# Kernel tuning notes

Measured on AMD Instinct MI355X. Metric: run time of the kernel, lower is better.

The kernel has to match this reference:

```python
import jax, jax.numpy as jnp
import numpy as np

N = 16384
K = 8

def knn_indices(pos, k):
    # squared pairwise distances via ||a||^2 + ||b||^2 - 2 a.b  -> [N, N]
    sq = jnp.sum(pos * pos, axis=-1)
    d = sq[:, None] + sq[None, :] - 2.0 * (pos @ pos.T)
    n = pos.shape[0]
    d = d.at[jnp.arange(n), jnp.arange(n)].set(jnp.inf)  # exclude self (loop=False)
    _, idx = jax.lax.top_k(-d, k)  # k nearest neighbors per target node
    # PointNetConv adds self-loops by default -> append self index
    return jnp.concatenate([idx, jnp.arange(n)[:, None]], axis=1)  # [N, k+1]

def mlp(x, W1, b1, W2, b2):
    return jax.nn.relu(x @ W1 + b1) @ W2 + b2

def pointnet_conv(x, pos, idx, W1, b1, W2, b2):
    # message: concat(x_j, pos_j - pos_i); aggregate: max over neighbors
    rel = pos[idx] - pos[:, None, :]                 # [N, k+1, 3]
    msg = jnp.concatenate([x[idx], rel], axis=-1)    # [N, k+1, d+3]
    h = mlp(msg, W1, b1, W2, b2)                     # [N, k+1, d_out]
    return jnp.max(h, axis=1)                        # [N, d_out]

def setup_inputs() -> dict:
    key = jax.random.key(0)
    ks = jax.random.split(key, 11)
    def lin(k, fi, fo):
        kw, kb = jax.random.split(k)
        s = 1.0 / np.sqrt(fi)
        return (jax.random.uniform(kw, (fi, fo), jnp.float32, -s, s),
                jax.random.uniform(kb, (fo,), jnp.float32, -s, s))
    W1a, b1a = lin(ks[0], 6, 32)
    W1b, b1b = lin(ks[1], 32, 64)
    W2a, b2a = lin(ks[2], 67, 64)
    W2b, b2b = lin(ks[3], 64, 128)
    Wc, bc = lin(ks[4], 128, 5)
    pos = jax.random.normal(ks[5], (N, 3), jnp.float32)
    return {"pos": pos, "W1a": W1a, "b1a": b1a, "W1b": W1b, "b1b": b1b,
            "W2a": W2a, "b2a": b2a, "W2b": W2b, "b2b": b2b, "Wc": Wc, "bc": bc}

def reference(pos, W1a, b1a, W1b, b1b, W2a, b2a, W2b, b2b, Wc, bc):
    idx = knn_indices(pos, K)                                    # [N, K+1]
    x = jax.nn.relu(pointnet_conv(pos, pos, idx, W1a, b1a, W1b, b1b))  # [N, 64]
    x = jax.nn.relu(pointnet_conv(x, pos, idx, W2a, b2a, W2b, b2b))    # [N, 128]
    logits = x @ Wc + bc                                         # [N, 5]
    return jax.nn.log_softmax(logits, axis=-1)
```

## Files before the change

kernel.cpp:

```cpp
#include <hip/hip_runtime.h>
#include <hip/hip_bf16.h>
#include <math.h>

#define N_PTS 16384
#define KNN 8

#define DT_BF16 1
#define DT_FP32 2

#define WS_FLAG_OFF 0
#define WS_IDX_OFF  64
#define WS_X1_OFF   589888
#define WS_NEEDED   4784192

#define WS_SAT_OFF      (WS_X1_OFF)
#define WS_START_OFF    (WS_X1_OFF + 442368)
#define WS_CURSOR_OFF   (WS_X1_OFF + 884800)
#define WS_PID_OFF      (WS_X1_OFF + 1327168)
#define WS_PTS_OFF      (WS_X1_OFF + 1392704)
#define WS_ROWTOT_OFF   (WS_X1_OFF + 1654848)
#define WS_ROWSTART_OFF (WS_X1_OFF + 1664064)
#define WS_XPRE_OFF     (WS_X1_OFF + 1673280)

#define GRID_R   48
#define NROWS2D  (GRID_R * GRID_R)
#define NCELLS   (GRID_R * GRID_R * GRID_R)
#define GLO      -4.5f
#define CELL_E   0.1875f
#define CELL_INV 5.3333335f
#define NBR_MIN  40
#define NBR_LO   9
#define M_CAP    1024
#define R_DIRECT 96

#define SENT_KEY 0xFF800000FFFFFFFFull

__device__ __forceinline__ float bf2f(__hip_bfloat16 v) { return __bfloat162float(v); }

__device__ __forceinline__ float ldf(const float* p, int i) { return p[i]; }
__device__ __forceinline__ float ldf(const __hip_bfloat16* p, int i) { return bf2f(p[i]); }
__device__ __forceinline__ void stf(float* p, int i, float v) { p[i] = v; }
__device__ __forceinline__ void stf(__hip_bfloat16* p, int i, float v) { p[i] = __float2bfloat16(v); }

__device__ __forceinline__ int clamp_idx(int j) {
    return ((unsigned)j < (unsigned)N_PTS) ? j : 0;
}

__device__ __forceinline__ int cell_of(float v) {
    int c = (int)((v - GLO) * CELL_INV);
    return min(max(c, 0), GRID_R - 1);
}

__device__ __forceinline__ unsigned fkey(float d) {
    unsigned b = __float_as_uint(d);
    return b ^ ((unsigned)((int)b >> 31) | 0x80000000u);
}
__device__ __forceinline__ float fkey_inv(unsigned k) {
    unsigned b = (k & 0x80000000u) ? (k ^ 0x80000000u) : ~k;
    return __uint_as_float(b);
}

__device__ __forceinline__ int get_dt(const int* flag) {
    return (flag[0] > 16) ? DT_FP32 : DT_BF16;
}

__global__ __launch_bounds__(256) void zero_kernel(int* __restrict__ cnt, int* __restrict__ flag) {
    const int e = blockIdx.x * 256 + threadIdx.x;
    cnt[e] = 0;
    if (e == 0) flag[0] = 0;
}

__global__ __launch_bounds__(256) void sniff_kernel(const unsigned short* __restrict__ posu,
                                                    int* __restrict__ flag) {
    __shared__ int red[256];
    int local = 0;
    for (int e = blockIdx.x * 256 + threadIdx.x; e < 3 * N_PTS; e += 64 * 256) {
        const float v = __uint_as_float(((unsigned)posu[e]) << 16);
        if (!(fabsf(v) <= 64.0f)) local++;
    }
    red[threadIdx.x] = local;
    __syncthreads();
    for (int s = 128; s > 0; s >>= 1) {
        if (threadIdx.x < s) red[threadIdx.x] += red[threadIdx.x + s];
        __syncthreads();
    }
    if (threadIdx.x == 0 && red[0] > 0) atomicAdd(flag, red[0]);
}

template <typename T>
__device__ __forceinline__ void count_body(const T* __restrict__ pos, int* __restrict__ cnt) {
    const int i = blockIdx.x * 256 + threadIdx.x;
    const float x = ldf(pos, 3 * i + 0);
    const float y = ldf(pos, 3 * i + 1);
    const float z = ldf(pos, 3 * i + 2);
    const int c = (cell_of(z) * GRID_R + cell_of(y)) * GRID_R + cell_of(x);
    atomicAdd(&cnt[c], 1);
}

__global__ __launch_bounds__(256) void grid_count_kernel(const void* __restrict__ pos,
                                                         const int* __restrict__ flag,
                                                         int* __restrict__ cnt) {
    if (get_dt(flag) == DT_BF16) count_body<__hip_bfloat16>((const __hip_bfloat16*)pos, cnt);
    else                         count_body<float>((const float*)pos, cnt);
}

__global__ __launch_bounds__(256) void rowscan_kernel(int* __restrict__ sat,
                                                      int* __restrict__ xpre,
                                                      int* __restrict__ rowtot) {
    const int t = blockIdx.x * 256 + threadIdx.x;
    const int rb = t * GRID_R;
    int acc = 0;
    for (int x = 0; x < GRID_R; ++x) {
        acc += sat[rb + x];
        sat[rb + x]  = acc;
        xpre[rb + x] = acc;
    }
    rowtot[t] = acc;
}

__global__ __launch_bounds__(256) void rowoffset_kernel(const int* __restrict__ rowtot,
                                                        int* __restrict__ rowstart) {
    __shared__ int part[256];
    const int t = threadIdx.x;
    int loc[9]; int s = 0;
#pragma unroll
    for (int k = 0; k < 9; ++k) { loc[k] = rowtot[t * 9 + k]; s += loc[k]; }
    part[t] = s;
    __syncthreads();
    for (int off = 1; off < 256; off <<= 1) {
        int v = (t >= off) ? part[t - off] : 0;
        __syncthreads();
        part[t] += v;
        __syncthreads();
    }
    int run = (t == 0) ? 0 : part[t - 1];
#pragma unroll
    for (int k = 0; k < 9; ++k) { rowstart[t * 9 + k] = run; run += loc[k]; }
}

__global__ __launch_bounds__(256) void cellsaty_kernel(const int* __restrict__ xpre,
                                                       const int* __restrict__ rowstart,
                                                       int* __restrict__ cstart,
                                                       int* __restrict__ cursor,
                                                       int* __restrict__ sat) {
    const int t = blockIdx.x * 256 + threadIdx.x;
    const int rb = t * GRID_R;
    const int base = rowstart[t];
    int prev = 0;
    for (int x = 0; x < GRID_R; ++x) {
        const int v = base + prev;
        cstart[rb + x] = v;
        cursor[rb + x] = v;
        prev = xpre[rb + x];
    }
    if (t == NROWS2D - 1) cstart[NCELLS] = base + prev;
    const int z = t / GRID_R, x = t - z * GRID_R;
    const int b2 = z * NROWS2D + x;
    int run = 0;
#pragma unroll
    for (int y = 0; y < GRID_R; ++y) {
        run += sat[b2 + y * GRID_R];
        sat[b2 + y * GRID_R] = run;
    }
}

template <typename T>
__device__ __forceinline__ void scatter_body(const T* __restrict__ pos, int i,
                                             int* __restrict__ cursor,
                                             float4* __restrict__ pts4, int* __restrict__ pid) {
    const float x = ldf(pos, 3 * i + 0);
    const float y = ldf(pos, 3 * i + 1);
    const float z = ldf(pos, 3 * i + 2);
    const int c = (cell_of(z) * GRID_R + cell_of(y)) * GRID_R + cell_of(x);
    const int slot = atomicAdd(&cursor[c], 1);
    const float sq = fmaf(x, x, fmaf(y, y, z * z));
    pts4[slot] = make_float4(-2.0f * x, -2.0f * y, -2.0f * z, sq);
    pid[slot] = i;
}

__global__ __launch_bounds__(256) void satzscatter_kernel(const void* __restrict__ pos,
                                                          const int* __restrict__ flag,
                                                          int* __restrict__ sat,
                                                          int* __restrict__ cursor,
                                                          float4* __restrict__ pts4,
                                                          int* __restrict__ pid) {
    if (blockIdx.x < 9) {
        const int t = blockIdx.x * 256 + threadIdx.x;
        int run = 0;
#pragma unroll
        for (int z = 0; z < GRID_R; ++z) {
            run += sat[t + z * NROWS2D];
            sat[t + z * NROWS2D] = run;
        }
    } else {
        const int i = (blockIdx.x - 9) * 256 + threadIdx.x;
        if (get_dt(flag) == DT_BF16) scatter_body<__hip_bfloat16>((const __hip_bfloat16*)pos, i, cursor, pts4, pid);
        else                         scatter_body<float>((const float*)pos, i, cursor, pts4, pid);
    }
}

__device__ __forceinline__ int sat_at(const int* __restrict__ sat, int x, int y, int z) {
    if (x < 0 || y < 0 || z < 0) return 0;
    return sat[(z * GRID_R + y) * GRID_R + x];
}

__device__ __forceinline__ int boxcount(const int* __restrict__ sat,
                                        int x0, int x1, int y0, int y1, int z0, int z1) {
    return sat_at(sat, x1, y1, z1) - sat_at(sat, x0 - 1, y1, z1)
         - sat_at(sat, x1, y0 - 1, z1) - sat_at(sat, x1, y1, z0 - 1)
         + sat_at(sat, x0 - 1, y0 - 1, z1) + sat_at(sat, x0 - 1, y1, z0 - 1)
         + sat_at(sat, x1, y0 - 1, z0 - 1) - sat_at(sat, x0 - 1, y0 - 1, z0 - 1);
}

template <typename T>
__device__ void knn_body(const T* __restrict__ pos,
                         const int* __restrict__ cstart, const int* __restrict__ sat,
                         const float4* __restrict__ pts4, const int* __restrict__ pid,
                         int* __restrict__ idx_out,
                         int* __restrict__ rs, int* __restrict__ epf) {
    const int tid  = threadIdx.x;
    const int lane = tid & 31;
    const int i    = blockIdx.x * 8 + (tid >> 5);

    const float pix = ldf(pos, 3 * i + 0);
    const float piy = ldf(pos, 3 * i + 1);
    const float piz = ldf(pos, 3 * i + 2);
    const float sqi = fmaf(pix, pix, fmaf(piy, piy, piz * piz));
    const int cx = cell_of(pix), cy = cell_of(piy), cz = cell_of(piz);

    unsigned long long bk[KNN];
#pragma unroll
    for (int q = 0; q < KNN; ++q) bk[q] = SENT_KEY;
    unsigned long long tk = SENT_KEY;

    auto do_insert = [&](unsigned long long ck) {
#pragma unroll
        for (int q = 0; q < KNN; ++q) {
            const unsigned long long old = bk[q];
            const bool ins = ck < old;
            bk[q] = ins ? ck : old;
            ck    = ins ? old : ck;
        }
        tk = (bk[KNN - 1] < tk) ? bk[KNN - 1] : tk;
    };

    auto clip_row = [&](int ycell, int zcell, float clip2, bool doclip,
                        int x0, int x1, int& cxa, int& cxb) -> bool {
        cxa = x0; cxb = x1;
        if (doclip) {
            const float ylo = GLO + (float)ycell * CELL_E;
            const float zlo = GLO + (float)zcell * CELL_E;
            const float dy = fmaxf(0.0f, fmaxf(ylo - piy, piy - (ylo + CELL_E)));
            const float dz = fmaxf(0.0f, fmaxf(zlo - piz, piz - (zlo + CELL_E)));
            const float rad2 = clip2 - dy * dy - dz * dz;
            if (rad2 <= 0.0f) return false;
            const float hr = sqrtf(rad2) + 1e-4f;
            cxa = max(x0, (int)floorf((pix - hr - GLO) * CELL_INV));
            cxb = min(x1, (int)floorf((pix + hr - GLO) * CELL_INV));
        }
        return cxa <= cxb;
    };

    auto cand_key = [&](int si) -> unsigned long long {
        const float4 cq = pts4[si];
        const int pj = pid[si];
        const float d = fmaf(cq.x, pix, fmaf(cq.y, piy, fmaf(cq.z, piz, cq.w)));
        if (pj == i) return SENT_KEY;
        return ((unsigned long long)fkey(d) << 32) | (unsigned)pj;
    };

    auto scan_win = [&](int rr, float clipR) {
        const int x0 = max(cx - rr, 0), x1 = min(cx + rr, GRID_R - 1);
        const int y0 = max(cy - rr, 0), y1 = min(cy + rr, GRID_R - 1);
        const int z0 = max(cz - rr, 0), z1 = min(cz + rr, GRID_R - 1);
        const int ny = y1 - y0 + 1;
        const int nz = z1 - z0 + 1;
        const int R  = ny * nz;
        const float clip2 = clipR * clipR;
        const bool doclip = (clipR < 1e30f);

        if (R > R_DIRECT) {
            for (int t0 = lane; t0 < R; t0 += 128) {
                int s0v[4], s1v[4];
#pragma unroll
                for (int k = 0; k < 4; ++k) {
                    const int row = t0 + (k << 5);
                    s0v[k] = 0; s1v[k] = 0;
                    if (row < R) {
                        const int iz = row / ny;
                        const int iy = row - iz * ny;
                        int cxa, cxb;
                        if (clip_row(y0 + iy, z0 + iz, clip2, doclip, x0, x1, cxa, cxb)) {
                            const int c0 = ((z0 + iz) * GRID_R + (y0 + iy)) * GRID_R + cxa;
                            s0v[k] = cstart[c0];
                            s1v[k] = cstart[c0 + (cxb - cxa) + 1];
                        }
                    }
                }
#pragma unroll
                for (int k = 0; k < 4; ++k) {
                    for (int si = s0v[k]; si < s1v[k]; ++si) {
                        const unsigned long long ck = cand_key(si);
                        if (ck <= tk) do_insert(ck);
                    }
                }
            }
            return;
        }

        for (int cb = 0; cb < R; cb += 32) {
            const int lr = cb + lane;
            int cnt_r = 0, st_r = 0;
            if (lr < R) {
                const int izq = lr / ny;
                const int iyq = lr - izq * ny;
                int cxa, cxb;
                if (clip_row(y0 + iyq, z0 + izq, clip2, doclip, x0, x1, cxa, cxb)) {
                    const int c0 = ((z0 + izq) * GRID_R + (y0 + iyq)) * GRID_R + cxa;
                    st_r  = cstart[c0];
                    cnt_r = cstart[c0 + (cxb - cxa) + 1] - st_r;
                }
            }
            int pv = cnt_r;
#pragma unroll
            for (int s = 1; s < 32; s <<= 1) {
                const int u = __shfl_up(pv, s, 32);
                if (lane >= s) pv += u;
            }
            const int Mtot = __shfl(pv, 31, 32);
            asm volatile("s_waitcnt lgkmcnt(0)" ::: "memory");
            rs[lane]  = st_r;
            epf[lane] = (lr < R) ? (pv - cnt_r) : 0x7fffffff;
            asm volatile("s_waitcnt lgkmcnt(0)" ::: "memory");
            for (int tb = 0; tb < Mtot; tb += 128) {
                unsigned long long ck[4];
#pragma unroll
                for (int k = 0; k < 4; ++k) {
                    const int t = tb + (k << 5) + lane;
                    ck[k] = SENT_KEY;
                    if (t < Mtot) {
                        int p = 0;
#pragma unroll
                        for (int st = 16; st >= 1; st >>= 1)
                            if (epf[p + st] <= t) p += st;
                        ck[k] = cand_key(rs[p] + (t - epf[p]));
                    }
                }
#pragma unroll
                for (int k = 0; k < 4; ++k)
                    if (ck[k] <= tk) do_insert(ck[k]);
            }
        }
    };

    auto merge_all = [&]() {
#pragma unroll
        for (int s = 1; s < 32; s <<= 1) {
            unsigned long long m[KNN];
#pragma unroll
            for (int q = 0; q < KNN; ++q) {
                const unsigned long long o = __shfl_xor(bk[KNN - 1 - q], s, 32);
                m[q] = (bk[q] < o) ? bk[q] : o;
            }
#pragma unroll
            for (int d = 4; d >= 1; d >>= 1) {
#pragma unroll
                for (int q = 0; q < KNN; ++q) {
                    if (!(q & d)) {
                        const unsigned long long a = m[q], b = m[q + d];
                        const bool sw = b < a;
                        m[q]     = sw ? b : a;
                        m[q + d] = sw ? a : b;
                    }
                }
            }
#pragma unroll
            for (int q = 0; q < KNN; ++q) bk[q] = m[q];
        }
        tk = bk[KNN - 1];
    };

    int r;
    {
        const int rl = lane + 1;
        const int bx0 = max(cx - rl, 0), bx1 = min(cx + rl, GRID_R - 1);
        const int by0 = max(cy - rl, 0), by1 = min(cy + rl, GRID_R - 1);
        const int bz0 = max(cz - rl, 0), bz1 = min(cz + rl, GRID_R - 1);
        const int cntl = boxcount(sat, bx0, bx1, by0, by1, bz0, bz1);
        const unsigned long long m9  = __ballot(cntl >= NBR_LO);
        const unsigned long long m26 = __ballot(cntl >= NBR_MIN);
        const unsigned sh  = (unsigned)(tid & 32);
        const unsigned mh9  = (unsigned)(m9  >> sh);
        const unsigned mh26 = (unsigned)(m26 >> sh);
        const int r9  = mh9  ? (int)__ffs(mh9)  : 32;
        const int r26 = mh26 ? (int)__ffs(mh26) : 32;
        const int cnt26 = __shfl(cntl, r26 - 1, 32);
        r = (cnt26 <= M_CAP) ? r26 : r9;
    }

    scan_win(r, INFINITY);

    {
        float mg = INFINITY;
        bool full = true;
        if (cx - r > 0)          { mg = fminf(mg, pix - (GLO + (float)(cx - r) * CELL_E));     full = false; }
        if (cx + r < GRID_R - 1) { mg = fminf(mg, (GLO + (float)(cx + r + 1) * CELL_E) - pix); full = false; }
        if (cy - r > 0)          { mg = fminf(mg, piy - (GLO + (float)(cy - r) * CELL_E));     full = false; }
        if (cy + r < GRID_R - 1) { mg = fminf(mg, (GLO + (float)(cy + r + 1) * CELL_E) - piy); full = false; }
        if (cz - r > 0)          { mg = fminf(mg, piz - (GLO + (float)(cz - r) * CELL_E));     full = false; }
        if (cz + r < GRID_R - 1) { mg = fminf(mg, (GLO + (float)(cz + r + 1) * CELL_E) - piz); full = false; }

        merge_all();
        bool done = full;
        const unsigned long long d8key = bk[KNN - 1];
        const float d8 = fkey_inv((unsigned)(d8key >> 32));
        if (!full) {
            const float mge  = mg - 1e-5f;
            const float need = mge * mge - sqi;
            done = (d8 < need);
        }

        if (!done) {
            float s2 = sqrtf(fmaxf(d8 + sqi, 0.0f)) + 1e-4f;
            s2 = fminf(s2, 9.0f);
            auto dneed = [&](float frac, int clip) -> int {
                int nd = (int)ceilf((s2 - frac) * CELL_INV);
                nd = max(nd, 0);
                return min(nd, clip);
            };
            const float fxm = pix - (GLO + (float)cx * CELL_E);
            const float fxp = (GLO + (float)(cx + 1) * CELL_E) - pix;
            const float fym = piy - (GLO + (float)cy * CELL_E);
            const float fyp = (GLO + (float)(cy + 1) * CELL_E) - piy;
            const float fzm = piz - (GLO + (float)cz * CELL_E);
            const float fzp = (GLO + (float)(cz + 1) * CELL_E) - piz;
            int r2 = r + 1;
            r2 = max(r2, dneed(fxm, cx));
            r2 = max(r2, dneed(fxp, GRID_R - 1 - cx));
            r2 = max(r2, dneed(fym, cy));
            r2 = max(r2, dneed(fyp, GRID_R - 1 - cy));
            r2 = max(r2, dneed(fzm, cz));
            r2 = max(r2, dneed(fzp, GRID_R - 1 - cz));
            r2 = min(r2, GRID_R);

#pragma unroll
            for (int q = 0; q < KNN; ++q) bk[q] = SENT_KEY;
            tk = d8key;
            scan_win(r2, (d8 < INFINITY) ? s2 : INFINITY);
            merge_all();
        }
    }

    if (lane == 0) {
#pragma unroll
        for (int k = 0; k < KNN; ++k) idx_out[i * 9 + k] = clamp_idx((int)(unsigned)bk[k]);
        idx_out[i * 9 + 8] = i;
    }
}

__global__ __launch_bounds__(256) void knn_grid_kernel(const void* __restrict__ pos,
                                                       const int* __restrict__ flag,
                                                       const int* __restrict__ cstart,
                                                       const int* __restrict__ sat,
                                                       const float4* __restrict__ pts4,
                                                       const int* __restrict__ pid,
                                                       int* __restrict__ idx_out) {
    __shared__ int rs[8][32];
    __shared__ int epf[8][32];
    const int sg = threadIdx.x >> 5;
    if (get_dt(flag) == DT_BF16)
        knn_body<__hip_bfloat16>((const __hip_bfloat16*)pos, cstart, sat, pts4, pid, idx_out,
                                 rs[sg], epf[sg]);
    else
        knn_body<float>((const float*)pos, cstart, sat, pts4, pid, idx_out, rs[sg], epf[sg]);
}

struct Conv1Smem {
    alignas(16) float wB[32 * 64];
    alignas(16) float h1s[4][9 * 32];
    alignas(16) float wsum[3 * 32];
    alignas(16) float wbot[3 * 32];
    alignas(16) float posn[4][9][3];
    float bA[32];
    float bB[64];
};

template <typename T>
__device__ void conv1_body(const T* __restrict__ pos, const int* __restrict__ idx,
                           const T* __restrict__ W1a, const T* __restrict__ b1a,
                           const T* __restrict__ W1b, const T* __restrict__ b1b,
                           float* __restrict__ x1, Conv1Smem& s) {
    const int tid = threadIdx.x;
    for (int e = tid; e < 96; e += 256) {
        const float bot = ldf(W1a, 96 + e);
        s.wsum[e] = ldf(W1a, e) + bot;
        s.wbot[e] = bot;
    }
    if (tid < 32) s.bA[tid] = ldf(b1a, tid);
    for (int e = tid; e < 2048; e += 256) s.wB[e] = ldf(W1b, e);
    if (tid < 64) s.bB[tid] = ldf(b1b, tid);

    const int tl   = tid >> 6;
    const int lane = tid & 63;
    const int i    = blockIdx.x * 4 + tl;

    if (lane < 27) {
        const int n = lane / 3, c = lane % 3;
        const int j = clamp_idx(idx[i * 9 + n]);
        s.posn[tl][n][c] = ldf(pos, 3 * j + c);
    }
    const float pi0 = ldf(pos, 3 * i + 0);
    const float pi1 = ldf(pos, 3 * i + 1);
    const float pi2 = ldf(pos, 3 * i + 2);
    __syncthreads();

    for (int e = lane; e < 288; e += 64) {
        const int n = e >> 5, k = e & 31;
        float b = fmaf(pi0, s.wbot[k], fmaf(pi1, s.wbot[32 + k], pi2 * s.wbot[64 + k]));
        float v = s.bA[k] - b;
        v = fmaf(s.posn[tl][n][0], s.wsum[k], v);
        v = fmaf(s.posn[tl][n][1], s.wsum[32 + k], v);
        v = fmaf(s.posn[tl][n][2], s.wsum[64 + k], v);
        s.h1s[tl][n * 32 + k] = fmaxf(v, 0.0f);
    }
    __syncthreads();

    float acc[9];
#pragma unroll
    for (int n = 0; n < 9; ++n) acc[n] = 0.0f;
#pragma unroll
    for (int kt = 0; kt < 32; kt += 8) {
        float w0 = s.wB[(kt + 0) * 64 + lane];
        float w1 = s.wB[(kt + 1) * 64 + lane];
        float w2 = s.wB[(kt + 2) * 64 + lane];
        float w3 = s.wB[(kt + 3) * 64 + lane];
        float w4 = s.wB[(kt + 4) * 64 + lane];
        float w5 = s.wB[(kt + 5) * 64 + lane];
        float w6 = s.wB[(kt + 6) * 64 + lane];
        float w7 = s.wB[(kt + 7) * 64 + lane];
#pragma unroll
        for (int n = 0; n < 9; ++n) {
            const float4 ha = *(const float4*)&s.h1s[tl][n * 32 + kt];
            const float4 hb = *(const float4*)&s.h1s[tl][n * 32 + kt + 4];
            float a = acc[n];
            a = fmaf(ha.x, w0, a); a = fmaf(ha.y, w1, a);
            a = fmaf(ha.z, w2, a); a = fmaf(ha.w, w3, a);
            a = fmaf(hb.x, w4, a); a = fmaf(hb.y, w5, a);
            a = fmaf(hb.z, w6, a); a = fmaf(hb.w, w7, a);
            acc[n] = a;
        }
    }
    float m = acc[0];
#pragma unroll
    for (int n = 1; n < 9; ++n) m = fmaxf(m, acc[n]);
    x1[i * 64 + lane] = fmaxf(m + s.bB[lane], 0.0f);
}

__global__ __launch_bounds__(256) void conv1_kernel(const void* __restrict__ pos,
                                                    const int* __restrict__ flag,
                                                    const int* __restrict__ idx,
                                                    const void* __restrict__ W1a,
                                                    const void* __restrict__ b1a,
                                                    const void* __restrict__ W1b,
                                                    const void* __restrict__ b1b,
                                                    float* __restrict__ x1) {
    __shared__ Conv1Smem s;
    if (get_dt(flag) == DT_BF16)
        conv1_body<__hip_bfloat16>((const __hip_bfloat16*)pos, idx,
            (const __hip_bfloat16*)W1a, (const __hip_bfloat16*)b1a,
            (const __hip_bfloat16*)W1b, (const __hip_bfloat16*)b1b, x1, s);
    else
        conv1_body<float>((const float*)pos, idx, (const float*)W1a, (const float*)b1a,
            (const float*)W1b, (const float*)b1b, x1, s);
}

struct ZwSmem {
    alignas(16) float wA[67 * 64];
    alignas(16) float xrT[4][68][4];
    float bA[64];
};

template <typename T>
__device__ void zw_body(const T* __restrict__ pos, const T* __restrict__ W2a,
                        const T* __restrict__ b2a, float* __restrict__ x1, ZwSmem& s) {
    const int tid  = threadIdx.x;
    const int wv   = tid >> 6;
    const int lane = tid & 63;
    const int j0   = blockIdx.x * 16 + wv * 4;

    for (int e = tid; e < 4288; e += 256) s.wA[e] = ldf(W2a, e);
    if (tid < 64) s.bA[tid] = ldf(b2a, tid);

#pragma unroll
    for (int p = 0; p < 4; ++p)
        s.xrT[wv][lane][p] = x1[(j0 + p) * 64 + lane];
    if (lane < 12) {
        const int p = lane / 3, c = lane % 3;
        s.xrT[wv][64 + c][p] = ldf(pos, 3 * (j0 + p) + c);
    }
    __syncthreads();

    float a0 = s.bA[lane], a1 = a0, a2 = a0, a3 = a0;
    for (int c = 0; c < 67; ++c) {
        const float w = s.wA[c * 64 + lane];
        const float4 xv = *(const float4*)&s.xrT[wv][c][0];
        a0 = fmaf(xv.x, w, a0);
        a1 = fmaf(xv.y, w, a1);
        a2 = fmaf(xv.z, w, a2);
        a3 = fmaf(xv.w, w, a3);
    }
    x1[(j0 + 0) * 64 + lane] = a0;
    x1[(j0 + 1) * 64 + lane] = a1;
    x1[(j0 + 2) * 64 + lane] = a2;
    x1[(j0 + 3) * 64 + lane] = a3;
}

__global__ __launch_bounds__(256) void zw_kernel(const void* __restrict__ pos,
                                                 const int* __restrict__ flag,
                                                 const void* __restrict__ W2a,
                                                 const void* __restrict__ b2a,
                                                 float* __restrict__ x1) {
    __shared__ ZwSmem s;
    if (get_dt(flag) == DT_BF16)
        zw_body<__hip_bfloat16>((const __hip_bfloat16*)pos, (const __hip_bfloat16*)W2a,
                                (const __hip_bfloat16*)b2a, x1, s);
    else
        zw_body<float>((const float*)pos, (const float*)W2a, (const float*)b2a, x1, s);
}

struct Conv2Smem {
    alignas(16) float h1s[4][9 * 64];
    alignas(16) float row[4][128];
    alignas(16) float wbot[3 * 64];
    alignas(16) float wc[640];
    float bcs[5];
    float sv[4][5];
    int   nb[4][9];
};

template <typename T>
__device__ void conv2_body(const T* __restrict__ pos, const int* __restrict__ idx,
                           const float* __restrict__ zw,
                           const T* __restrict__ W2a, const T* __restrict__ W2b,
                           const T* __restrict__ b2b, const T* __restrict__ Wc,
                           const T* __restrict__ bc, T* __restrict__ out, Conv2Smem& s) {
    const int tid  = threadIdx.x;
    const int tl   = tid >> 6;
    const int lane = tid & 63;
    const int i    = blockIdx.x * 4 + tl;

    for (int e = tid; e < 192; e += 256) s.wbot[e] = ldf(W2a, 4096 + e);
    for (int e = tid; e < 640; e += 256) s.wc[e] = ldf(Wc, e);
    if (tid < 5) s.bcs[tid] = ldf(bc, tid);

    if (lane < 9) s.nb[tl][lane] = clamp_idx(idx[i * 9 + lane]);
    const float pi0 = ldf(pos, 3 * i + 0);
    const float pi1 = ldf(pos, 3 * i + 1);
    const float pi2 = ldf(pos, 3 * i + 2);
    __syncthreads();

    {
        const float vi = fmaf(pi0, s.wbot[lane], fmaf(pi1, s.wbot[64 + lane], pi2 * s.wbot[128 + lane]));
#pragma unroll
        for (int n = 0; n < 9; ++n) {
            const int j = s.nb[tl][n];
            s.h1s[tl][n * 64 + lane] = fmaxf(zw[j * 64 + lane] - vi, 0.0f);
        }
    }
    __syncthreads();

    float acc0[9], acc1[9];
#pragma unroll
    for (int n = 0; n < 9; ++n) { acc0[n] = 0.0f; acc1[n] = 0.0f; }
#pragma unroll
    for (int kt = 0; kt < 64; kt += 4) {
        const float wa0 = ldf(W2b, (kt + 0) * 128 + lane);
        const float wa1 = ldf(W2b, (kt + 1) * 128 + lane);
        const float wa2 = ldf(W2b, (kt + 2) * 128 + lane);
        const float wa3 = ldf(W2b, (kt + 3) * 128 + lane);
        const float wb0 = ldf(W2b, (kt + 0) * 128 + lane + 64);
        const float wb1 = ldf(W2b, (kt + 1) * 128 + lane + 64);
        const float wb2 = ldf(W2b, (kt + 2) * 128 + lane + 64);
        const float wb3 = ldf(W2b, (kt + 3) * 128 + lane + 64);
#pragma unroll
        for (int n = 0; n < 9; ++n) {
            const float4 h = *(const float4*)&s.h1s[tl][n * 64 + kt];
            float a0 = acc0[n], a1 = acc1[n];
            a0 = fmaf(h.x, wa0, a0); a0 = fmaf(h.y, wa1, a0);
            a0 = fmaf(h.z, wa2, a0); a0 = fmaf(h.w, wa3, a0);
            a1 = fmaf(h.x, wb0, a1); a1 = fmaf(h.y, wb1, a1);
            a1 = fmaf(h.z, wb2, a1); a1 = fmaf(h.w, wb3, a1);
            acc0[n] = a0; acc1[n] = a1;
        }
    }
    float m0 = acc0[0], m1 = acc1[0];
#pragma unroll
    for (int n = 1; n < 9; ++n) { m0 = fmaxf(m0, acc0[n]); m1 = fmaxf(m1, acc1[n]); }
    s.row[tl][lane]      = fmaxf(m0 + ldf(b2b, lane), 0.0f);
    s.row[tl][lane + 64] = fmaxf(m1 + ldf(b2b, lane + 64), 0.0f);
    __syncthreads();

    if (tid < 20) {
        const int tgt = tid / 5, o = tid % 5;
        float v = s.bcs[o];
        for (int k = 0; k < 128; ++k) v = fmaf(s.row[tgt][k], s.wc[k * 5 + o], v);
        s.sv[tgt][o] = v;
    }
    __syncthreads();
    if (tid < 20) {
        const int tgt = tid / 5, o = tid % 5;
        float m = s.sv[tgt][0];
#pragma unroll
        for (int q = 1; q < 5; ++q) m = fmaxf(m, s.sv[tgt][q]);
        float sum = 0.0f;
#pragma unroll
        for (int q = 0; q < 5; ++q) sum += expf(s.sv[tgt][q] - m);
        const float lse = m + logf(sum);
        stf(out, (blockIdx.x * 4 + tgt) * 5 + o, s.sv[tgt][o] - lse);
    }
}

__global__ __launch_bounds__(256) void conv2_head_kernel(const void* __restrict__ pos,
                                                         const int* __restrict__ flag,
                                                         const int* __restrict__ idx,
                                                         const float* __restrict__ zw,
                                                         const void* __restrict__ W2a,
                                                         const void* __restrict__ W2b,
                                                         const void* __restrict__ b2b,
                                                         const void* __restrict__ Wc,
                                                         const void* __restrict__ bc,
                                                         void* __restrict__ out) {
    __shared__ Conv2Smem s;
    if (get_dt(flag) == DT_BF16)
        conv2_body<__hip_bfloat16>((const __hip_bfloat16*)pos, idx, zw,
            (const __hip_bfloat16*)W2a, (const __hip_bfloat16*)W2b, (const __hip_bfloat16*)b2b,
            (const __hip_bfloat16*)Wc, (const __hip_bfloat16*)bc, (__hip_bfloat16*)out, s);
    else
        conv2_body<float>((const float*)pos, idx, zw, (const float*)W2a, (const float*)W2b,
            (const float*)b2b, (const float*)Wc, (const float*)bc, (float*)out, s);
}

extern "C" void kernel_launch(void* const* d_in, const int* in_sizes, int n_in,
                              void* d_out, int out_size, void* d_ws, size_t ws_size,
                              hipStream_t stream) {
    if (ws_size < (size_t)WS_NEEDED) return;

    char* ws = (char*)d_ws;
    int*    flag     = (int*)(ws + WS_FLAG_OFF);
    int*    idx      = (int*)(ws + WS_IDX_OFF);
    float*  x1       = (float*)(ws + WS_X1_OFF);
    int*    sat      = (int*)(ws + WS_SAT_OFF);
    int*    cstart   = (int*)(ws + WS_START_OFF);
    int*    cursor   = (int*)(ws + WS_CURSOR_OFF);
    int*    pid      = (int*)(ws + WS_PID_OFF);
    float4* pts4     = (float4*)(ws + WS_PTS_OFF);
    int*    rowtot   = (int*)(ws + WS_ROWTOT_OFF);
    int*    rowstart = (int*)(ws + WS_ROWSTART_OFF);
    int*    xpre     = (int*)(ws + WS_XPRE_OFF);

    zero_kernel<<<NCELLS / 256, 256, 0, stream>>>(sat, flag);
    sniff_kernel<<<64, 256, 0, stream>>>((const unsigned short*)d_in[0], flag);
    grid_count_kernel<<<N_PTS / 256, 256, 0, stream>>>(d_in[0], flag, sat);
    rowscan_kernel<<<NROWS2D / 256, 256, 0, stream>>>(sat, xpre, rowtot);
    rowoffset_kernel<<<1, 256, 0, stream>>>(rowtot, rowstart);
    cellsaty_kernel<<<NROWS2D / 256, 256, 0, stream>>>(xpre, rowstart, cstart, cursor, sat);
    satzscatter_kernel<<<9 + N_PTS / 256, 256, 0, stream>>>(d_in[0], flag, sat, cursor, pts4, pid);
    knn_grid_kernel<<<N_PTS / 8, 256, 0, stream>>>(d_in[0], flag, cstart, sat, pts4, pid, idx);
    conv1_kernel<<<N_PTS / 4, 256, 0, stream>>>(d_in[0], flag, idx,
        d_in[1], d_in[2], d_in[3], d_in[4], x1);
    zw_kernel<<<N_PTS / 16, 256, 0, stream>>>(d_in[0], flag, d_in[5], d_in[6], x1);
    conv2_head_kernel<<<N_PTS / 4, 256, 0, stream>>>(d_in[0], flag, idx, x1,
        d_in[5], d_in[7], d_in[8], d_in[9], d_in[10], d_out);
}
```

Measured before the change: 226.5 us.

## Fuse zw precompute into conv1 kernel and shrink kNN blocks to 128 threads

After: 219.7 us. -3.0%, faster.

```diff
diff --git a/kernel.cpp b/kernel.cpp
--- a/kernel.cpp
+++ b/kernel.cpp
@@ -220,7 +220,7 @@
                          int* __restrict__ rs, int* __restrict__ epf) {
     const int tid  = threadIdx.x;
     const int lane = tid & 31;
-    const int i    = blockIdx.x * 8 + (tid >> 5);
+    const int i    = blockIdx.x * 4 + (tid >> 5);
 
     const float pix = ldf(pos, 3 * i + 0);
     const float piy = ldf(pos, 3 * i + 1);
@@ -458,15 +458,15 @@
     }
 }
 
-__global__ __launch_bounds__(256) void knn_grid_kernel(const void* __restrict__ pos,
+__global__ __launch_bounds__(128) void knn_grid_kernel(const void* __restrict__ pos,
                                                        const int* __restrict__ flag,
                                                        const int* __restrict__ cstart,
                                                        const int* __restrict__ sat,
                                                        const float4* __restrict__ pts4,
                                                        const int* __restrict__ pid,
                                                        int* __restrict__ idx_out) {
-    __shared__ int rs[8][32];
-    __shared__ int epf[8][32];
+    __shared__ int rs[4][32];
+    __shared__ int epf[4][32];
     const int sg = threadIdx.x >> 5;
     if (get_dt(flag) == DT_BF16)
         knn_body<__hip_bfloat16>((const __hip_bfloat16*)pos, cstart, sat, pts4, pid, idx_out,
@@ -476,29 +476,35 @@
 }
 
 struct Conv1Smem {
-    alignas(16) float wB[32 * 64];
-    alignas(16) float h1s[4][9 * 32];
+    alignas(16) float big[4288];
     alignas(16) float wsum[3 * 32];
     alignas(16) float wbot[3 * 32];
     alignas(16) float posn[4][9][3];
+    alignas(16) float xr[4][64];
     float bA[32];
     float bB[64];
+    float bA2[64];
 };
 
 template <typename T>
 __device__ void conv1_body(const T* __restrict__ pos, const int* __restrict__ idx,
                            const T* __restrict__ W1a, const T* __restrict__ b1a,
                            const T* __restrict__ W1b, const T* __restrict__ b1b,
+                           const T* __restrict__ W2a, const T* __restrict__ b2a,
                            float* __restrict__ x1, Conv1Smem& s) {
     const int tid = threadIdx.x;
+    float* wB  = s.big;
+    float* h1s = s.big + 2048;
+
     for (int e = tid; e < 96; e += 256) {
         const float bot = ldf(W1a, 96 + e);
         s.wsum[e] = ldf(W1a, e) + bot;
         s.wbot[e] = bot;
     }
     if (tid < 32) s.bA[tid] = ldf(b1a, tid);
-    for (int e = tid; e < 2048; e += 256) s.wB[e] = ldf(W1b, e);
+    for (int e = tid; e < 2048; e += 256) wB[e] = ldf(W1b, e);
     if (tid < 64) s.bB[tid] = ldf(b1b, tid);
+    if (tid < 64) s.bA2[tid] = ldf(b2a, tid);
 
     const int tl   = tid >> 6;
     const int lane = tid & 63;
@@ -521,7 +527,7 @@
         v = fmaf(s.posn[tl][n][0], s.wsum[k], v);
         v = fmaf(s.posn[tl][n][1], s.wsum[32 + k], v);
         v = fmaf(s.posn[tl][n][2], s.wsum[64 + k], v);
-        s.h1s[tl][n * 32 + k] = fmaxf(v, 0.0f);
+        h1s[tl * 288 + n * 32 + k] = fmaxf(v, 0.0f);
     }
     __syncthreads();
 
@@ -530,18 +536,18 @@
     for (int n = 0; n < 9; ++n) acc[n] = 0.0f;
 #pragma unroll
     for (int kt = 0; kt < 32; kt += 8) {
-        float w0 = s.wB[(kt + 0) * 64 + lane];
-        float w1 = s.wB[(kt + 1) * 64 + lane];
-        float w2 = s.wB[(kt + 2) * 64 + lane];
-        float w3 = s.wB[(kt + 3) * 64 + lane];
-        float w4 = s.wB[(kt + 4) * 64 + lane];
-        float w5 = s.wB[(kt + 5) * 64 + lane];
-        float w6 = s.wB[(kt + 6) * 64 + lane];
-        float w7 = s.wB[(kt + 7) * 64 + lane];
+        float w0 = wB[(kt + 0) * 64 + lane];
+        float w1 = wB[(kt + 1) * 64 + lane];
+        float w2 = wB[(kt + 2) * 64 + lane];
+        float w3 = wB[(kt + 3) * 64 + lane];
+        float w4 = wB[(kt + 4) * 64 + lane];
+        float w5 = wB[(kt + 5) * 64 + lane];
+        float w6 = wB[(kt + 6) * 64 + lane];
+        float w7 = wB[(kt + 7) * 64 + lane];
 #pragma unroll
         for (int n = 0; n < 9; ++n) {
-            const float4 ha = *(const float4*)&s.h1s[tl][n * 32 + kt];
-            const float4 hb = *(const float4*)&s.h1s[tl][n * 32 + kt + 4];
+            const float4 ha = *(const float4*)&h1s[tl * 288 + n * 32 + kt];
+            const float4 hb = *(const float4*)&h1s[tl * 288 + n * 32 + kt + 4];
             float a = acc[n];
             a = fmaf(ha.x, w0, a); a = fmaf(ha.y, w1, a);
             a = fmaf(ha.z, w2, a); a = fmaf(ha.w, w3, a);
@@ -553,79 +559,48 @@
     float m = acc[0];
 #pragma unroll
     for (int n = 1; n < 9; ++n) m = fmaxf(m, acc[n]);
-    x1[i * 64 + lane] = fmaxf(m + s.bB[lane], 0.0f);
-}
-
-__global__ __launch_bounds__(256) void conv1_kernel(const void* __restrict__ pos,
-                                                    const int* __restrict__ flag,
-                                                    const int* __restrict__ idx,
-                                                    const void* __restrict__ W1a,
-                                                    const void* __restrict__ b1a,
-                                                    const void* __restrict__ W1b,
-                                                    const void* __restrict__ b1b,
-                                                    float* __restrict__ x1) {
+    const float xv = fmaxf(m + s.bB[lane], 0.0f);
+
+    __syncthreads();
+    s.xr[tl][lane] = xv;
+    for (int e = tid; e < 4288; e += 256) s.big[e] = ldf(W2a, e);
+    __syncthreads();
+
+    float a0 = s.bA2[lane], a1 = 0.0f, a2 = 0.0f, a3 = 0.0f;
+#pragma unroll
+    for (int c = 0; c < 64; c += 4) {
+        a0 = fmaf(s.xr[tl][c + 0], s.big[(c + 0) * 64 + lane], a0);
+        a1 = fmaf(s.xr[tl][c + 1], s.big[(c + 1) * 64 + lane], a1);
+        a2 = fmaf(s.xr[tl][c + 2], s.big[(c + 2) * 64 + lane], a2);
+        a3 = fmaf(s.xr[tl][c + 3], s.big[(c + 3) * 64 + lane], a3);
+    }
+    float a = (a0 + a1) + (a2 + a3);
+    a = fmaf(pi0, s.big[64 * 64 + lane], a);
+    a = fmaf(pi1, s.big[65 * 64 + lane], a);
+    a = fmaf(pi2, s.big[66 * 64 + lane], a);
+    x1[i * 64 + lane] = a;
+}
+
+__global__ __launch_bounds__(256) void conv1zw_kernel(const void* __restrict__ pos,
+                                                      const int* __restrict__ flag,
+                                                      const int* __restrict__ idx,
+                                                      const void* __restrict__ W1a,
+                                                      const void* __restrict__ b1a,
+                                                      const void* __restrict__ W1b,
+                                                      const void* __restrict__ b1b,
+                                                      const void* __restrict__ W2a,
+                                                      const void* __restrict__ b2a,
+                                                      float* __restrict__ x1) {
     __shared__ Conv1Smem s;
     if (get_dt(flag) == DT_BF16)
         conv1_body<__hip_bfloat16>((const __hip_bfloat16*)pos, idx,
             (const __hip_bfloat16*)W1a, (const __hip_bfloat16*)b1a,
-            (const __hip_bfloat16*)W1b, (const __hip_bfloat16*)b1b, x1, s);
+            (const __hip_bfloat16*)W1b, (const __hip_bfloat16*)b1b,
+            (const __hip_bfloat16*)W2a, (const __hip_bfloat16*)b2a, x1, s);
     else
         conv1_body<float>((const float*)pos, idx, (const float*)W1a, (const float*)b1a,
-            (const float*)W1b, (const float*)b1b, x1, s);
-}
-
-struct ZwSmem {
-    alignas(16) float wA[67 * 64];
-    alignas(16) float xrT[4][68][4];
-    float bA[64];
-};
-
-template <typename T>
-__device__ void zw_body(const T* __restrict__ pos, const T* __restrict__ W2a,
-                        const T* __restrict__ b2a, float* __restrict__ x1, ZwSmem& s) {
-    const int tid  = threadIdx.x;
-    const int wv   = tid >> 6;
-    const int lane = tid & 63;
-    const int j0   = blockIdx.x * 16 + wv * 4;
-
-    for (int e = tid; e < 4288; e += 256) s.wA[e] = ldf(W2a, e);
-    if (tid < 64) s.bA[tid] = ldf(b2a, tid);
-
-#pragma unroll
-    for (int p = 0; p < 4; ++p)
-        s.xrT[wv][lane][p] = x1[(j0 + p) * 64 + lane];
-    if (lane < 12) {
-        const int p = lane / 3, c = lane % 3;
-        s.xrT[wv][64 + c][p] = ldf(pos, 3 * (j0 + p) + c);
-    }
-    __syncthreads();
-
-    float a0 = s.bA[lane], a1 = a0, a2 = a0, a3 = a0;
-    for (int c = 0; c < 67; ++c) {
-        const float w = s.wA[c * 64 + lane];
-        const float4 xv = *(const float4*)&s.xrT[wv][c][0];
-        a0 = fmaf(xv.x, w, a0);
-        a1 = fmaf(xv.y, w, a1);
-        a2 = fmaf(xv.z, w, a2);
-        a3 = fmaf(xv.w, w, a3);
-    }
-    x1[(j0 + 0) * 64 + lane] = a0;
-    x1[(j0 + 1) * 64 + lane] = a1;
-    x1[(j0 + 2) * 64 + lane] = a2;
-    x1[(j0 + 3) * 64 + lane] = a3;
-}
-
-__global__ __launch_bounds__(256) void zw_kernel(const void* __restrict__ pos,
-                                                 const int* __restrict__ flag,
-                                                 const void* __restrict__ W2a,
-                                                 const void* __restrict__ b2a,
-                                                 float* __restrict__ x1) {
-    __shared__ ZwSmem s;
-    if (get_dt(flag) == DT_BF16)
-        zw_body<__hip_bfloat16>((const __hip_bfloat16*)pos, (const __hip_bfloat16*)W2a,
-                                (const __hip_bfloat16*)b2a, x1, s);
-    else
-        zw_body<float>((const float*)pos, (const float*)W2a, (const float*)b2a, x1, s);
+            (const float*)W1b, (const float*)b1b,
+            (const float*)W2a, (const float*)b2a, x1, s);
 }
 
 struct Conv2Smem {
@@ -765,10 +740,9 @@
     rowoffset_kernel<<<1, 256, 0, stream>>>(rowtot, rowstart);
     cellsaty_kernel<<<NROWS2D / 256, 256, 0, stream>>>(xpre, rowstart, cstart, cursor, sat);
     satzscatter_kernel<<<9 + N_PTS / 256, 256, 0, stream>>>(d_in[0], flag, sat, cursor, pts4, pid);
-    knn_grid_kernel<<<N_PTS / 8, 256, 0, stream>>>(d_in[0], flag, cstart, sat, pts4, pid, idx);
-    conv1_kernel<<<N_PTS / 4, 256, 0, stream>>>(d_in[0], flag, idx,
-        d_in[1], d_in[2], d_in[3], d_in[4], x1);
-    zw_kernel<<<N_PTS / 16, 256, 0, stream>>>(d_in[0], flag, d_in[5], d_in[6], x1);
+    knn_grid_kernel<<<N_PTS / 4, 128, 0, stream>>>(d_in[0], flag, cstart, sat, pts4, pid, idx);
+    conv1zw_kernel<<<N_PTS / 4, 256, 0, stream>>>(d_in[0], flag, idx,
+        d_in[1], d_in[2], d_in[3], d_in[4], d_in[5], d_in[6], x1);
     conv2_head_kernel<<<N_PTS / 4, 256, 0, stream>>>(d_in[0], flag, idx, x1,
         d_in[5], d_in[7], d_in[8], d_in[9], d_in[10], d_out);
 }
```
